# Optimization experiments

Hardware: AMD Instinct MI355X
Metric: run time of the kernel (lower is better)

Reference implementation:

```python
import jax, jax.numpy as jnp
import numpy as np

B, N, D = 64, 1024, 512
H, LD = 8, 64            # num_heads, linear_hidden_dim (H*LD == D)
HIDDEN = 4 * D           # ffn_multiply = 4.0
NB = 128                 # number of timestamp buckets
EPS = 1e-6
TS_SCALE = NB / 14.0     # log1p(1e6) ~ 13.8 -> buckets span [0, NB]


def rms_norm(x, eps=EPS):
    return x * jax.lax.rsqrt(jnp.mean(x * x, axis=-1, keepdims=True) + eps)


def setup_inputs() -> dict:
    key = jax.random.key(0)
    ks = jax.random.split(key, 8)
    lengths = np.linspace(256, N, B).astype(np.int64)
    x_offsets = jnp.asarray(np.concatenate([[0], np.cumsum(lengths)]), dtype=jnp.int64)
    T = int(lengths.sum())
    x = jax.random.normal(ks[0], (T, D), dtype=jnp.float32)
    all_timestamps = jnp.sort(jax.random.randint(ks[1], (B, N), 0, 10**6, dtype=jnp.int64), axis=1)
    invalid_attn_mask = jnp.tril(jnp.ones((N, N), jnp.float32))  # causal
    uv = jax.random.normal(ks[2], (D, 3 * H * LD), dtype=jnp.float32) * 0.02
    pos_w = jax.random.normal(ks[3], (2 * N - 1,), dtype=jnp.float32) * 0.02
    ts_w = jax.random.normal(ks[4], (NB + 1,), dtype=jnp.float32) * 0.02
    w_ams = jax.random.normal(ks[5], (2 * H * LD, D), dtype=jnp.float32) * 0.02
    w1 = jax.random.normal(ks[6], (D, HIDDEN), dtype=jnp.float32) * 0.02
    w2 = jax.random.normal(ks[7], (HIDDEN, D), dtype=jnp.float32) * 0.02
    return {"x": x, "x_offsets": x_offsets, "all_timestamps": all_timestamps,
            "invalid_attn_mask": invalid_attn_mask, "uv": uv, "pos_w": pos_w,
            "ts_w": ts_w, "w_ams": w_ams, "w1": w1, "w2": w2}


def reference(x, x_offsets, all_timestamps, invalid_attn_mask, uv, pos_w, ts_w, w_ams, w1, w2):
    T = x.shape[0]
    # RMSNorm (no learned scale, matches F.rms_norm with no weight) + fused proj + SiLU
    proj = jax.nn.silu(rms_norm(x) @ uv)                       # [T, 3*H*LD]
    u, v = proj[:, :2 * H * LD], proj[:, 2 * H * LD:]          # [T,2HD'], [T,HD']
    # jagged -> padded dense
    tok = jnp.arange(T)
    seg = jnp.searchsorted(x_offsets, tok, side="right") - 1   # batch id per token
    pos = tok - x_offsets[seg]                                  # position within sequence
    padded_v = jnp.zeros((B, N, H * LD), v.dtype).at[seg, pos].set(v).reshape(B, N, H, LD)
    # positional relative bias (batch-independent)
    rel = jnp.arange(N)[:, None] - jnp.arange(N)[None, :]
    pos_attn = pos_w[rel + N - 1] * invalid_attn_mask           # [N,N]
    # temporal relative bias: log-bucketized |t_i - t_j|
    dt = jnp.abs(all_timestamps[:, :, None] - all_timestamps[:, None, :]).astype(jnp.float32)
    bucket = jnp.clip(jnp.floor(jnp.log1p(dt) * TS_SCALE), 0, NB).astype(jnp.int32)
    ts_attn = ts_w[bucket] * invalid_attn_mask[None]            # [B,N,N]
    # two-stream bias 'attention' (no softmax)
    out_pos = jnp.einsum("nm,bmhd->bnhd", pos_attn, padded_v)
    out_ts = jnp.einsum("bnm,bmhd->bnhd", ts_attn, padded_v)
    combined = jnp.concatenate([out_pos, out_ts], axis=-1).reshape(B, N, 2 * H * LD)
    attn_out = combined[seg, pos]                               # dense -> jagged, [T, 2*H*LD]
    # gated norm + multistage FFN with residuals
    ams = u * rms_norm(attn_out)
    h = x + ams @ w_ams
    out = h + jax.nn.silu(rms_norm(h) @ w1) @ w2
    return out
```

## Files before the change

kernel.cpp:

```cpp
#include <hip/hip_runtime.h>
#include <cmath>


using u16 = unsigned short;
using u8  = unsigned char;

typedef __bf16 bf16x8 __attribute__((ext_vector_type(8)));
typedef float  f32x4  __attribute__((ext_vector_type(4)));

#define TS_SCALE_F (float)(128.0 / 14.0)

__device__ __forceinline__ u16 f2b(float f) {
  unsigned u = __float_as_uint(f);
  unsigned r = 0x7FFFu + ((u >> 16) & 1u);
  return (u16)((u + r) >> 16);
}
__device__ __forceinline__ float b2f(u16 v) {
  return __uint_as_float(((unsigned)v) << 16);
}
__device__ __forceinline__ bf16x8 as_frag(uint4 r) {
  union { uint4 u; bf16x8 v; } c; c.u = r; return c.v;
}

__device__ __forceinline__ void gload_lds16(const u16* g, u16* l) {
  __builtin_amdgcn_global_load_lds(
      (const __attribute__((address_space(1))) unsigned int*)g,
      (__attribute__((address_space(3))) unsigned int*)l, 16, 0, 0);
}

__device__ __forceinline__ size_t ts_base_u8(int b, int nt) {
  return (size_t)b * 589824 + (size_t)(nt * (nt + 1) / 2) * 16384;
}

__global__ __launch_bounds__(256) void wprep(
    const float* __restrict__ W, u16* __restrict__ Wp, int K, int N)
{
  const int p = blockIdx.x, s = blockIdx.y;
  const int t = threadIdx.x;
  size_t base = ((size_t)p * (K >> 5) + s) * 4096;
  const int e0 = t * 16;
  u16 o[16];
#pragma unroll
  for (int i = 0; i < 16; ++i) {
    int e = e0 + i;
    int kb = e >> 10, r = e & 1023, c = r >> 3, ke = r & 7;
    o[i] = f2b(W[(size_t)(s * 32 + kb * 8 + ke) * N + p * 128 + c]);
  }
  *(uint4*)(Wp + base + e0)     = *(uint4*)o;
  *(uint4*)(Wp + base + e0 + 8) = *(uint4*)(o + 8);
}

#define EPI_SILU_BF16 0
#define EPI_ADD_F32   1
#define AM_BF16   0
#define AM_F32S   1
#define AM_BF16SM 2

template <int EPI, int AMODE>
__global__ __launch_bounds__(256, 2) void gemm_bf16(
    const u16* __restrict__ A, const float* __restrict__ Af,
    const float* __restrict__ inv, const u16* __restrict__ U, int ustride,
    const u16* __restrict__ Wp, void* __restrict__ C,
    const float* __restrict__ ADD, int M, int N, int K)
{
  __shared__ u16 lA[2][128 * 40];
  __shared__ u16 lB[2][4096];

  const int tid  = threadIdx.x;
  const int c0b  = blockIdx.x;
  const int t0   = blockIdx.y * 128;
  const int c0   = c0b * 128;
  const int wave = tid >> 6, lane = tid & 63;
  const int wr   = (wave >> 1) * 64, wc = (wave & 1) * 64;
  const int l15  = lane & 15, l4 = lane >> 4;

  f32x4 z = {0.f, 0.f, 0.f, 0.f};
  f32x4 acc[4][4];
#pragma unroll
  for (int m = 0; m < 4; ++m)
#pragma unroll
    for (int j = 0; j < 4; ++j) acc[m][j] = z;

  const int ar = tid >> 1, ak = (tid & 1) * 16;
  const int row = t0 + ar;
  const bool arow_ok = row < M;
  float rinv = 0.f;
  if (AMODE != AM_BF16 && arow_ok) rinv = inv[row];
  const u16*   ab = (AMODE != AM_F32S) ? A + (size_t)row * K + ak : nullptr;
  const float* af = (AMODE == AM_F32S) ? Af + (size_t)row * K + ak : nullptr;
  const u16*   um = (AMODE == AM_BF16SM) ? U + (size_t)row * ustride + ak : nullptr;

  uint4 pr[4];
  const uint4 z4 = make_uint4(0, 0, 0, 0);

  auto loadA = [&](int k0) {
    if (!arow_ok) { pr[0] = z4; pr[1] = z4; pr[2] = z4; pr[3] = z4; return; }
    if constexpr (AMODE == AM_BF16) {
      pr[0] = *(const uint4*)(ab + k0);
      pr[1] = *(const uint4*)(ab + k0 + 8);
    } else if constexpr (AMODE == AM_F32S) {
      pr[0] = *(const uint4*)(af + k0);
      pr[1] = *(const uint4*)(af + k0 + 4);
      pr[2] = *(const uint4*)(af + k0 + 8);
      pr[3] = *(const uint4*)(af + k0 + 12);
    } else {
      pr[0] = *(const uint4*)(ab + k0);
      pr[1] = *(const uint4*)(ab + k0 + 8);
      pr[2] = *(const uint4*)(um + k0);
      pr[3] = *(const uint4*)(um + k0 + 8);
    }
  };
  auto writeA = [&](u16* dst) {
    u16 tmp[16];
    if constexpr (AMODE == AM_BF16) {
      *(uint4*)tmp       = pr[0];
      *(uint4*)(tmp + 8) = pr[1];
    } else if constexpr (AMODE == AM_F32S) {
      const float* f = (const float*)pr;
#pragma unroll
      for (int i = 0; i < 16; ++i) tmp[i] = f2b(f[i] * rinv);
    } else {
      const u16* a = (const u16*)pr;
      const u16* u = (const u16*)(pr + 2);
#pragma unroll
      for (int i = 0; i < 16; ++i) tmp[i] = f2b(b2f(a[i]) * rinv * b2f(u[i]));
    }
    *(uint4*)(dst + ar * 40 + ak)     = *(uint4*)tmp;
    *(uint4*)(dst + ar * 40 + ak + 8) = *(uint4*)(tmp + 8);
  };

  const int ksteps = K >> 5;
  const u16* wsrc = Wp + (size_t)c0b * ksteps * 4096 + wave * 1024 + lane * 8;

  loadA(0);
  gload_lds16(wsrc,       &lB[0][wave * 1024]);
  gload_lds16(wsrc + 512, &lB[0][wave * 1024 + 512]);
  wsrc += 4096;
  writeA(&lA[0][0]);
  __syncthreads();

  int buf = 0;
  for (int s = 0; s < ksteps; ++s) {
    if (s + 1 < ksteps) {
      gload_lds16(wsrc,       &lB[buf ^ 1][wave * 1024]);
      gload_lds16(wsrc + 512, &lB[buf ^ 1][wave * 1024 + 512]);
      wsrc += 4096;
      loadA((s + 1) * 32);
    }
    const u16* lAc = &lA[buf][0];
    const u16* lBc = &lB[buf][0];
    bf16x8 afr[4], bfv[4];
#pragma unroll
    for (int m = 0; m < 4; ++m)
      afr[m] = as_frag(*(const uint4*)&lAc[(wr + m * 16 + l15) * 40 + l4 * 8]);
#pragma unroll
    for (int j = 0; j < 4; ++j)
      bfv[j] = as_frag(*(const uint4*)&lBc[(l4 << 10) + (wc + j * 16 + l15) * 8]);
#pragma unroll
    for (int m = 0; m < 4; ++m)
#pragma unroll
      for (int j = 0; j < 4; ++j)
        acc[m][j] = __builtin_amdgcn_mfma_f32_16x16x32_bf16(afr[m], bfv[j], acc[m][j], 0, 0, 0);
    if (s + 1 < ksteps) writeA(&lA[buf ^ 1][0]);
    __syncthreads();
    buf ^= 1;
  }

#pragma unroll
  for (int m = 0; m < 4; ++m) {
#pragma unroll
    for (int r = 0; r < 4; ++r) {
      int orow = t0 + wr + m * 16 + l4 * 4 + r;
      if (orow >= M) continue;
#pragma unroll
      for (int j = 0; j < 4; ++j) {
        int col = c0 + wc + j * 16 + l15;
        size_t idx = (size_t)orow * N + col;
        float y = acc[m][j][r];
        if constexpr (EPI == EPI_SILU_BF16) {
          float s = y / (1.f + __expf(-y));
          ((u16*)C)[idx] = f2b(s);
        } else {
          ((float*)C)[idx] = y + ADD[idx];
        }
      }
    }
  }
}

__global__ __launch_bounds__(128) void pos_scores(
    const float* __restrict__ pos_w, u16* __restrict__ pos_s)
{
  const int n = blockIdx.x;
  const int m0 = threadIdx.x * 8;
  u16 o[8];
#pragma unroll
  for (int i = 0; i < 8; ++i) {
    int m = m0 + i;
    float v = (m <= n) ? pos_w[n - m + 1023] : 0.f;
    o[i] = f2b(v);
  }
  *(uint4*)(pos_s + (size_t)n * 1024 + m0) = *(uint4*)o;
}

__global__ __launch_bounds__(256) void ts_buckets(
    const int* __restrict__ tstamp, u8* __restrict__ ts_s)
{
  const int nt = 7 - (blockIdx.x >> 6);
  const int b  = blockIdx.x & 63;
  const int W  = 128 * (nt + 1);
  const int n0 = nt * 128;
  const int tid = threadIdx.x;

  __shared__ int tsm[1024];
  for (int i = tid; i < W; i += 256) tsm[i] = tstamp[b * 1024 + i];
  __syncthreads();

  const int r = tid >> 1, h = tid & 1;
  const int n_abs = n0 + r;
  const int t_n = tstamp[b * 1024 + n_abs];
  const int half = W >> 1;
  const int c0 = h * half;
  u8* row = ts_s + ts_base_u8(b, nt) + (size_t)r * W + c0;

  for (int c = 0; c < half; c += 16) {
    u8 o[16];
#pragma unroll
    for (int i = 0; i < 16; ++i) {
      int m = c0 + c + i;
      int d = t_n - tsm[m];
      if (d < 0) d = -d;
      int bkt = (int)(log1pf((float)d) * TS_SCALE_F);
      bkt = bkt > 128 ? 128 : bkt;
      o[i] = (m <= n_abs) ? (u8)bkt : (u8)129;
    }
    *(uint4*)(row + c) = *(uint4*)o;
  }
}

__global__ __launch_bounds__(256, 1) void attn_gemm(
    const u16* __restrict__ proj,
    const int* __restrict__ xoff,
    const u16* __restrict__ pos_s,
    const u8*  __restrict__ tsU8,
    const float* __restrict__ ts_w,
    u16* __restrict__ attn_out,
    int Ttot)
{
  const int flat = blockIdx.x;
  const int nt = 7 - (flat >> 8);
  const int rem = flat & 255;
  const int b  = rem >> 2;
  const int ct = rem & 3;

  const int off = xoff[b];
  int len = xoff[b + 1] - off;
  if (len < 0) len = 0;
  if (len > 1024) len = 1024;
  if (off < 0 || off + len > Ttot) return;
  const int n0 = nt * 128;
  if (n0 >= len) return;
  const int c0 = ct * 128;
  const int W = 128 * (nt + 1);

  __shared__ u16 lP[128 * 40];
  __shared__ u16 lT[128 * 40];
  __shared__ u16 sV[4096];
  __shared__ float s_tsw[130];

  const int tid = threadIdx.x;
  if (tid < 130) s_tsw[tid] = (tid < 129) ? ts_w[tid] : 0.f;
  __syncthreads();

  const int wave = tid >> 6, lane = tid & 63;
  const int wr = (wave >> 1) * 64, wc = (wave & 1) * 64;
  const int l15 = lane & 15, l4 = lane >> 4;

  f32x4 z = {0.f, 0.f, 0.f, 0.f};
  f32x4 accP[4][4], accT[4][4];
#pragma unroll
  for (int m = 0; m < 4; ++m)
#pragma unroll
    for (int j = 0; j < 4; ++j) { accP[m][j] = z; accT[m][j] = z; }

  const int ar = tid >> 1, ak = (tid & 1) * 16;
  const u16* pRow = pos_s + (size_t)(n0 + ar) * 1024 + ak;
  const u8*  tRow = tsU8 + ts_base_u8(b, nt) + (size_t)ar * W + ak;
  const int vk = tid >> 3, vc = (tid & 7) * 16;

  const int mEnd = (n0 + 128 < len) ? (n0 + 128) : len;

  for (int m0 = 0; m0 < mEnd; m0 += 32) {
    {
      int mm = m0 + vk;
      uint4 v0 = make_uint4(0, 0, 0, 0), v1 = v0;
      if (mm < len) {
        const u16* src = proj + (size_t)(off + mm) * 1536 + 1024 + c0 + vc;
        v0 = *(const uint4*)src;
        v1 = *(const uint4*)(src + 8);
      }
      u16 tmp[16];
      *(uint4*)tmp       = v0;
      *(uint4*)(tmp + 8) = v1;
      const int kb = vk >> 3, ke = vk & 7;
#pragma unroll
      for (int i = 0; i < 16; ++i) {
        int col = vc + i;
        int o2 = (kb * 2048 + col * 16 + ke * 2) ^ (((col >> 3) & 7) << 4);
        *(u16*)((char*)sV + o2) = tmp[i];
      }
    }
    {
      uint4 p0 = *(const uint4*)(pRow + m0);
      uint4 p1 = *(const uint4*)(pRow + m0 + 8);
      uint4 tb = *(const uint4*)(tRow + m0);
      u16 tt[16];
      const u8* bp = (const u8*)&tb;
#pragma unroll
      for (int i = 0; i < 16; ++i) tt[i] = f2b(s_tsw[bp[i]]);
      int wb = ar * 40 + ak;
      *(uint4*)&lP[wb]     = p0;
      *(uint4*)&lP[wb + 8] = p1;
      *(uint4*)&lT[wb]     = *(uint4*)tt;
      *(uint4*)&lT[wb + 8] = *(uint4*)(tt + 8);
    }
    __syncthreads();

    bf16x8 ap[4], at[4], bv[4];
#pragma unroll
    for (int m = 0; m < 4; ++m) {
      ap[m] = as_frag(*(const uint4*)&lP[(wr + m * 16 + l15) * 40 + l4 * 8]);
      at[m] = as_frag(*(const uint4*)&lT[(wr + m * 16 + l15) * 40 + l4 * 8]);
    }
#pragma unroll
    for (int j = 0; j < 4; ++j) {
      int col = wc + j * 16 + l15;
      int o2 = (l4 * 2048 + col * 16) ^ (((col >> 3) & 7) << 4);
      bv[j] = as_frag(*(const uint4*)((char*)sV + o2));
    }
#pragma unroll
    for (int m = 0; m < 4; ++m)
#pragma unroll
      for (int j = 0; j < 4; ++j) {
        accP[m][j] = __builtin_amdgcn_mfma_f32_16x16x32_bf16(ap[m], bv[j], accP[m][j], 0, 0, 0);
        accT[m][j] = __builtin_amdgcn_mfma_f32_16x16x32_bf16(at[m], bv[j], accT[m][j], 0, 0, 0);
      }
    __syncthreads();
  }

#pragma unroll
  for (int m = 0; m < 4; ++m)
#pragma unroll
    for (int r = 0; r < 4; ++r) {
      int n = n0 + wr + m * 16 + l4 * 4 + r;
      if (n >= len) continue;
      size_t t = (size_t)(off + n);
#pragma unroll
      for (int j = 0; j < 4; ++j) {
        int hd = c0 + wc + j * 16 + l15;
        int colP = ((hd >> 6) << 7) + (hd & 63);
        attn_out[t * 1024 + colP]      = f2b(accP[m][j][r]);
        attn_out[t * 1024 + colP + 64] = f2b(accT[m][j][r]);
      }
    }
}

template <int D, bool F32IN>
__global__ __launch_bounds__(256) void row_ss(
    const void* __restrict__ in, float* __restrict__ inv, int T)
{
  const int row = blockIdx.x * 4 + (threadIdx.x >> 6);
  const int lane = threadIdx.x & 63;
  if (row >= T) return;
  float ss = 0.f;
  if constexpr (F32IN) {
    const float* r = (const float*)in + (size_t)row * D;
#pragma unroll
    for (int i = lane * 4; i < D; i += 256) {
      float4 v = *(const float4*)(r + i);
      ss += v.x * v.x + v.y * v.y + v.z * v.z + v.w * v.w;
    }
  } else {
    const u16* r = (const u16*)in + (size_t)row * D;
#pragma unroll
    for (int i = lane * 8; i < D; i += 512) {
      uint4 v = *(const uint4*)(r + i);
      const u16* q = (const u16*)&v;
#pragma unroll
      for (int k = 0; k < 8; ++k) { float f = b2f(q[k]); ss += f * f; }
    }
  }
#pragma unroll
  for (int o = 32; o > 0; o >>= 1) ss += __shfl_down(ss, o, 64);
  if (lane == 0) inv[row] = rsqrtf(ss / (float)D + 1e-6f);
}

extern "C" void kernel_launch(void* const* d_in, const int* in_sizes, int n_in,
                              void* d_out, int out_size, void* d_ws, size_t ws_size,
                              hipStream_t stream)
{
  const float* x      = (const float*)d_in[0];
  const int*   xoff   = (const int*)d_in[1];
  const int*   tstamp = (const int*)d_in[2];
  const float* uv     = (const float*)d_in[4];
  const float* pos_w  = (const float*)d_in[5];
  const float* ts_w   = (const float*)d_in[6];
  const float* w_ams  = (const float*)d_in[7];
  const float* w1     = (const float*)d_in[8];
  const float* w2     = (const float*)d_in[9];
  const int T = in_sizes[0] / 512;

  char* ws = (char*)d_ws;
  size_t o = 0;
  auto take = [&](size_t bytes) { size_t r = o; o += (bytes + 255) & ~(size_t)255; return r; };

  u16* uvb    = (u16*)(ws + take((size_t)512 * 1536 * 2));
  u16* wamsb  = (u16*)(ws + take((size_t)1024 * 512 * 2));
  u16* w1b    = (u16*)(ws + take((size_t)512 * 2048 * 2));
  u16* w2b    = (u16*)(ws + take((size_t)2048 * 512 * 2));
  u16* posS   = (u16*)(ws + take((size_t)1024 * 1024 * 2));

  size_t o_ts   = take((size_t)64 * 589824);
  size_t o_attn = take((size_t)T * 1024 * 2);
  size_t o_proj = take((size_t)T * 1536 * 2);
  float* invX = (float*)(ws + take((size_t)T * 4));
  float* invA = (float*)(ws + take((size_t)T * 4));
  float* invH = (float*)(ws + take((size_t)T * 4));

  u8*  tsU8  = (u8*)(ws + o_ts);
  u16* attnS = (u16*)(ws + o_attn);
  u16* proj  = (u16*)(ws + o_proj);
  u16* mid   = (u16*)(ws + o_ts);
  float* h   = (float*)d_out;

  if (ws_size < o) return;

  wprep<<<dim3(12, 16), 256, 0, stream>>>(uv,    uvb,   512,  1536);
  wprep<<<dim3(4, 32),  256, 0, stream>>>(w_ams, wamsb, 1024, 512);
  wprep<<<dim3(16, 16), 256, 0, stream>>>(w1,    w1b,   512,  2048);
  wprep<<<dim3(4, 64),  256, 0, stream>>>(w2,    w2b,   2048, 512);

  pos_scores<<<1024, 128, 0, stream>>>(pos_w, posS);
  ts_buckets<<<512, 256, 0, stream>>>(tstamp, tsU8);

  row_ss<512, true><<<(T + 3) / 4, 256, 0, stream>>>(x, invX, T);

  dim3 g1(12, (T + 127) / 128);
  gemm_bf16<EPI_SILU_BF16, AM_F32S><<<g1, 256, 0, stream>>>(
      nullptr, x, invX, nullptr, 0, uvb, proj, nullptr, T, 1536, 512);

  attn_gemm<<<64 * 32, 256, 0, stream>>>(proj, xoff, posS, tsU8, ts_w, attnS, T);

  row_ss<1024, false><<<(T + 3) / 4, 256, 0, stream>>>(attnS, invA, T);

  dim3 g3(4, (T + 127) / 128);
  gemm_bf16<EPI_ADD_F32, AM_BF16SM><<<g3, 256, 0, stream>>>(
      attnS, nullptr, invA, proj, 1536, wamsb, h, x, T, 512, 1024);

  row_ss<512, true><<<(T + 3) / 4, 256, 0, stream>>>(h, invH, T);

  dim3 g4(16, (T + 127) / 128);
  gemm_bf16<EPI_SILU_BF16, AM_F32S><<<g4, 256, 0, stream>>>(
      nullptr, h, invH, nullptr, 0, w1b, mid, nullptr, T, 2048, 512);

  dim3 g5(4, (T + 127) / 128);
  gemm_bf16<EPI_ADD_F32, AM_BF16><<<g5, 256, 0, stream>>>(
      mid, nullptr, nullptr, nullptr, 0, w2b, h, h, T, 512, 2048);
}
```

Baseline: 930.4 us.

## Remap GEMM blocks per XCD and drop LDS double buffering

Flattens the GEMM grid to 1D and remaps block indices so that consecutive work tiles (sharing the same row tile of A) land on the same XCD, improving L2 reuse across column blocks. It also removes the double-buffered LDS pipeline: each k-step now loads A and B, syncs, computes, and syncs again. This halves LDS usage, which could raise occupancy, but loses the overlap of global loads with MFMA compute.

```diff
diff --git a/kernel.cpp b/kernel.cpp
--- a/kernel.cpp
+++ b/kernel.cpp
@@ -61,15 +61,20 @@
     const u16* __restrict__ A, const float* __restrict__ Af,
     const float* __restrict__ inv, const u16* __restrict__ U, int ustride,
     const u16* __restrict__ Wp, void* __restrict__ C,
-    const float* __restrict__ ADD, int M, int N, int K)
-{
-  __shared__ u16 lA[2][128 * 40];
-  __shared__ u16 lB[2][4096];
+    const float* __restrict__ ADD, int M, int N, int K, int ncb)
+{
+  __shared__ u16 lA[128 * 40];
+  __shared__ u16 lB[4096];
+
+  const int nblk = gridDim.x;
+  const int q = nblk >> 3, r = nblk & 7;
+  const int xcd = blockIdx.x & 7, li = blockIdx.x >> 3;
+  const int work = xcd * q + (xcd < r ? xcd : r) + li;
+  const int c0b = work % ncb;
+  const int t0  = (work / ncb) * 128;
+  const int c0  = c0b * 128;
 
   const int tid  = threadIdx.x;
-  const int c0b  = blockIdx.x;
-  const int t0   = blockIdx.y * 128;
-  const int c0   = c0b * 128;
   const int wave = tid >> 6, lane = tid & 63;
   const int wr   = (wave >> 1) * 64, wc = (wave & 1) * 64;
   const int l15  = lane & 15, l4 = lane >> 4;
@@ -90,12 +95,16 @@
   const float* af = (AMODE == AM_F32S) ? Af + (size_t)row * K + ak : nullptr;
   const u16*   um = (AMODE == AM_BF16SM) ? U + (size_t)row * ustride + ak : nullptr;
 
-  uint4 pr[4];
-  const uint4 z4 = make_uint4(0, 0, 0, 0);
-
-  auto loadA = [&](int k0) {
-    if (!arow_ok) { pr[0] = z4; pr[1] = z4; pr[2] = z4; pr[3] = z4; return; }
-    if constexpr (AMODE == AM_BF16) {
+  const int ksteps = K >> 5;
+  const u16* wsrc = Wp + (size_t)c0b * ksteps * 4096 + wave * 1024 + lane * 8;
+  u16* ldsb = &lB[wave * 1024];
+
+  for (int s = 0; s < ksteps; ++s) {
+    const int k0 = s * 32;
+    uint4 pr[4];
+    const uint4 z4 = make_uint4(0, 0, 0, 0);
+    if (!arow_ok) { pr[0] = z4; pr[1] = z4; pr[2] = z4; pr[3] = z4; }
+    else if constexpr (AMODE == AM_BF16) {
       pr[0] = *(const uint4*)(ab + k0);
       pr[1] = *(const uint4*)(ab + k0 + 8);
     } else if constexpr (AMODE == AM_F32S) {
@@ -109,74 +118,55 @@
       pr[2] = *(const uint4*)(um + k0);
       pr[3] = *(const uint4*)(um + k0 + 8);
     }
-  };
-  auto writeA = [&](u16* dst) {
-    u16 tmp[16];
-    if constexpr (AMODE == AM_BF16) {
-      *(uint4*)tmp       = pr[0];
-      *(uint4*)(tmp + 8) = pr[1];
-    } else if constexpr (AMODE == AM_F32S) {
-      const float* f = (const float*)pr;
-#pragma unroll
-      for (int i = 0; i < 16; ++i) tmp[i] = f2b(f[i] * rinv);
-    } else {
-      const u16* a = (const u16*)pr;
-      const u16* u = (const u16*)(pr + 2);
-#pragma unroll
-      for (int i = 0; i < 16; ++i) tmp[i] = f2b(b2f(a[i]) * rinv * b2f(u[i]));
-    }
-    *(uint4*)(dst + ar * 40 + ak)     = *(uint4*)tmp;
-    *(uint4*)(dst + ar * 40 + ak + 8) = *(uint4*)(tmp + 8);
-  };
-
-  const int ksteps = K >> 5;
-  const u16* wsrc = Wp + (size_t)c0b * ksteps * 4096 + wave * 1024 + lane * 8;
-
-  loadA(0);
-  gload_lds16(wsrc,       &lB[0][wave * 1024]);
-  gload_lds16(wsrc + 512, &lB[0][wave * 1024 + 512]);
-  wsrc += 4096;
-  writeA(&lA[0][0]);
-  __syncthreads();
-
-  int buf = 0;
-  for (int s = 0; s < ksteps; ++s) {
-    if (s + 1 < ksteps) {
-      gload_lds16(wsrc,       &lB[buf ^ 1][wave * 1024]);
-      gload_lds16(wsrc + 512, &lB[buf ^ 1][wave * 1024 + 512]);
-      wsrc += 4096;
-      loadA((s + 1) * 32);
-    }
-    const u16* lAc = &lA[buf][0];
-    const u16* lBc = &lB[buf][0];
+    gload_lds16(wsrc,       ldsb);
+    gload_lds16(wsrc + 512, ldsb + 512);
+    wsrc += 4096;
+    {
+      u16 tmp[16];
+      if constexpr (AMODE == AM_BF16) {
+        *(uint4*)tmp       = pr[0];
+        *(uint4*)(tmp + 8) = pr[1];
+      } else if constexpr (AMODE == AM_F32S) {
+        const float* f = (const float*)pr;
+#pragma unroll
+        for (int i = 0; i < 16; ++i) tmp[i] = f2b(f[i] * rinv);
+      } else {
+        const u16* a = (const u16*)pr;
+        const u16* u = (const u16*)(pr + 2);
+#pragma unroll
+        for (int i = 0; i < 16; ++i) tmp[i] = f2b(b2f(a[i]) * rinv * b2f(u[i]));
+      }
+      *(uint4*)&lA[ar * 40 + ak]     = *(uint4*)tmp;
+      *(uint4*)&lA[ar * 40 + ak + 8] = *(uint4*)(tmp + 8);
+    }
+    __syncthreads();
+
     bf16x8 afr[4], bfv[4];
 #pragma unroll
     for (int m = 0; m < 4; ++m)
-      afr[m] = as_frag(*(const uint4*)&lAc[(wr + m * 16 + l15) * 40 + l4 * 8]);
+      afr[m] = as_frag(*(const uint4*)&lA[(wr + m * 16 + l15) * 40 + l4 * 8]);
 #pragma unroll
     for (int j = 0; j < 4; ++j)
-      bfv[j] = as_frag(*(const uint4*)&lBc[(l4 << 10) + (wc + j * 16 + l15) * 8]);
+      bfv[j] = as_frag(*(const uint4*)&lB[(l4 << 10) + (wc + j * 16 + l15) * 8]);
 #pragma unroll
     for (int m = 0; m < 4; ++m)
 #pragma unroll
       for (int j = 0; j < 4; ++j)
         acc[m][j] = __builtin_amdgcn_mfma_f32_16x16x32_bf16(afr[m], bfv[j], acc[m][j], 0, 0, 0);
-    if (s + 1 < ksteps) writeA(&lA[buf ^ 1][0]);
     __syncthreads();
-    buf ^= 1;
   }
 
 #pragma unroll
   for (int m = 0; m < 4; ++m) {
 #pragma unroll
-    for (int r = 0; r < 4; ++r) {
-      int orow = t0 + wr + m * 16 + l4 * 4 + r;
+    for (int rr = 0; rr < 4; ++rr) {
+      int orow = t0 + wr + m * 16 + l4 * 4 + rr;
       if (orow >= M) continue;
 #pragma unroll
       for (int j = 0; j < 4; ++j) {
         int col = c0 + wc + j * 16 + l15;
         size_t idx = (size_t)orow * N + col;
-        float y = acc[m][j][r];
+        float y = acc[m][j][rr];
         if constexpr (EPI == EPI_SILU_BF16) {
           float s = y / (1.f + __expf(-y));
           ((u16*)C)[idx] = f2b(s);
@@ -409,6 +399,7 @@
   const float* w1     = (const float*)d_in[8];
   const float* w2     = (const float*)d_in[9];
   const int T = in_sizes[0] / 512;
+  const int nrow = (T + 127) / 128;
 
   char* ws = (char*)d_ws;
   size_t o = 0;
@@ -445,25 +436,21 @@
 
   row_ss<512, true><<<(T + 3) / 4, 256, 0, stream>>>(x, invX, T);
 
-  dim3 g1(12, (T + 127) / 128);
-  gemm_bf16<EPI_SILU_BF16, AM_F32S><<<g1, 256, 0, stream>>>(
-      nullptr, x, invX, nullptr, 0, uvb, proj, nullptr, T, 1536, 512);
+  gemm_bf16<EPI_SILU_BF16, AM_F32S><<<12 * nrow, 256, 0, stream>>>(
+      nullptr, x, invX, nullptr, 0, uvb, proj, nullptr, T, 1536, 512, 12);
 
   attn_gemm<<<64 * 32, 256, 0, stream>>>(proj, xoff, posS, tsU8, ts_w, attnS, T);
 
   row_ss<1024, false><<<(T + 3) / 4, 256, 0, stream>>>(attnS, invA, T);
 
-  dim3 g3(4, (T + 127) / 128);
-  gemm_bf16<EPI_ADD_F32, AM_BF16SM><<<g3, 256, 0, stream>>>(
-      attnS, nullptr, invA, proj, 1536, wamsb, h, x, T, 512, 1024);
+  gemm_bf16<EPI_ADD_F32, AM_BF16SM><<<4 * nrow, 256, 0, stream>>>(
+      attnS, nullptr, invA, proj, 1536, wamsb, h, x, T, 512, 1024, 4);
 
   row_ss<512, true><<<(T + 3) / 4, 256, 0, stream>>>(h, invH, T);
 
-  dim3 g4(16, (T + 127) / 128);
-  gemm_bf16<EPI_SILU_BF16, AM_F32S><<<g4, 256, 0, stream>>>(
-      nullptr, h, invH, nullptr, 0, w1b, mid, nullptr, T, 2048, 512);
-
-  dim3 g5(4, (T + 127) / 128);
-  gemm_bf16<EPI_ADD_F32, AM_BF16><<<g5, 256, 0, stream>>>(
-      mid, nullptr, nullptr, nullptr, 0, w2b, h, h, T, 512, 2048);
-}
+  gemm_bf16<EPI_SILU_BF16, AM_F32S><<<16 * nrow, 256, 0, stream>>>(
+      nullptr, h, invH, nullptr, 0, w1b, mid, nullptr, T, 2048, 512, 16);
+
+  gemm_bf16<EPI_ADD_F32, AM_BF16><<<4 * nrow, 256, 0, stream>>>(
+      mid, nullptr, nullptr, nullptr, 0, w2b, h, h, T, 512, 2048, 4);
+}
```

After: 855.2 us. -8.1%, faster.
